# Optimization experiments

Hardware: AMD Instinct MI355X
Metric: run time of the kernel (lower is better)

The kernel has to match this reference:

```python
import jax, jax.numpy as jnp
import numpy as np

B, T, NW, NF = 4, 1, 1536, 16
N_CROSS = 400_000
N_EDGES = 1_600_000
C_OUT = 4
IN_DIM = 2 * NF + 2  # 34


def setup_inputs() -> dict:
    key = jax.random.key(0)
    ks = jax.random.split(key, 16)
    return {
        "first_wires": jax.random.normal(ks[0], (B, T, NW, NF), jnp.float32),
        "second_wires": jax.random.normal(ks[1], (B, T, NW, NF), jnp.float32),
        "crossings": jax.random.normal(ks[2], (N_CROSS, 2), jnp.float32),
        "bbox": jax.random.uniform(ks[3], (3,), jnp.float32) + 0.5,
        "edge_attr": jax.random.normal(ks[4], (N_EDGES, 4), jnp.float32),
        "indices": jax.random.randint(ks[5], (N_CROSS, 2), 0, NW),
        "edge_index": jax.random.randint(ks[6], (2, N_EDGES), 0, N_CROSS),
        "W": jax.random.normal(ks[7], (IN_DIM, C_OUT), jnp.float32) / np.sqrt(IN_DIM),
        "att_src": jax.random.normal(ks[8], (C_OUT,), jnp.float32),
        "att_dst": jax.random.normal(ks[9], (C_OUT,), jnp.float32),
        "W_e": jax.random.normal(ks[10], (4, C_OUT), jnp.float32) / 2.0,
        "att_edge": jax.random.normal(ks[11], (C_OUT,), jnp.float32),
        "bias": jnp.zeros((C_OUT,), jnp.float32),
        "w_mlp": jax.random.normal(ks[12], (C_OUT, 1), jnp.float32) / 2.0,
        "b_mlp": jnp.zeros((1,), jnp.float32),
    }


def reference(first_wires, second_wires, crossings, bbox, edge_attr,
              indices, edge_index, W, att_src, att_dst, W_e, att_edge,
              bias, w_mlp, b_mlp):
    b, t = first_wires.shape[0], first_wires.shape[1]
    n = indices.shape[0]
    # fill_window: gather wire features for each crossing and append normalized coords
    fw = first_wires[:, :, indices[:, 0], :]          # [B,T,N,NF]
    sw = second_wires[:, :, indices[:, 1], :]         # [B,T,N,NF]
    xc = crossings / jnp.linalg.norm(bbox)            # [N,2]
    xc = jnp.broadcast_to(xc[None, None], (b, t, n, 2))
    x = jnp.concatenate([fw, sw, xc], axis=-1)        # [B,T,N,2NF+2]
    x = x.reshape(b * t, n, -1)

    src, dst = edge_index[0], edge_index[1]
    h = x @ W                                          # [BT,N,C]
    a_e = (edge_attr @ W_e) @ att_edge                 # [E]

    def gat(hb):
        hs, hd = hb[src], hb[dst]                      # [E,C]
        logits = jax.nn.leaky_relu(hs @ att_src + hd @ att_dst + a_e, 0.2)
        m = jax.ops.segment_max(logits, dst, num_segments=n)
        ex = jnp.exp(logits - m[dst])
        den = jax.ops.segment_sum(ex, dst, num_segments=n)
        alpha = ex / (den[dst] + 1e-16)
        return jax.ops.segment_sum(alpha[:, None] * hs, dst, num_segments=n) + bias

    out = jax.vmap(gat)(h)                             # [BT,N,C]
    y = out @ w_mlp + b_mlp                            # [BT,N,1]
    return y.reshape(b, t, n, 1)
```

## Files before the change

kernel.cpp:

```cpp
#include <hip/hip_runtime.h>
#include <math.h>

#define BB 4
#define NWIRE 1536
#define NFEAT 16
#define BS 256
#define NBLK 256
#define DSHIFT 9
#define DPB (1 << DSHIFT)
#define MAXNB 1024

__global__ void k_wires(const float* __restrict__ fw, const float* __restrict__ sw,
                        const float* __restrict__ W, const float* __restrict__ att_src,
                        const float* __restrict__ att_dst, const float* __restrict__ wmlp,
                        float4* __restrict__ fwpre, float4* __restrict__ swpre) {
    int t = blockIdx.x * blockDim.x + threadIdx.x;
    if (t >= BB * NWIRE) return;
    const float* fp = fw + (size_t)t * NFEAT;
    const float* sp = sw + (size_t)t * NFEAT;
    float hf[4] = {0, 0, 0, 0}, hs[4] = {0, 0, 0, 0};
    #pragma unroll
    for (int k = 0; k < NFEAT; ++k) {
        float a = fp[k], b = sp[k];
        #pragma unroll
        for (int c = 0; c < 4; ++c) {
            hf[c] = fmaf(a, W[k * 4 + c], hf[c]);
            hs[c] = fmaf(b, W[(NFEAT + k) * 4 + c], hs[c]);
        }
    }
    float fs = 0, fd = 0, fq = 0, ss = 0, sd = 0, sq = 0;
    #pragma unroll
    for (int c = 0; c < 4; ++c) {
        float as = att_src[c], ad = att_dst[c], wm = wmlp[c];
        fs = fmaf(hf[c], as, fs); fd = fmaf(hf[c], ad, fd); fq = fmaf(hf[c], wm, fq);
        ss = fmaf(hs[c], as, ss); sd = fmaf(hs[c], ad, sd); sq = fmaf(hs[c], wm, sq);
    }
    fwpre[t] = make_float4(fs, fd, fq, 0.0f);
    swpre[t] = make_float4(ss, sd, sq, 0.0f);
}

__global__ void k_nodes(const int* __restrict__ indices, const float* __restrict__ crossings,
                        const float* __restrict__ bbox, const float* __restrict__ W,
                        const float* __restrict__ att_src, const float* __restrict__ att_dst,
                        const float* __restrict__ wmlp,
                        const float4* __restrict__ fwpre, const float4* __restrict__ swpre,
                        float4* __restrict__ srcdat4, float4* __restrict__ dstdat4, int n) {
    int i = blockIdx.x * blockDim.x + threadIdx.x;
    if (i >= n) return;
    float inv = rsqrtf(bbox[0] * bbox[0] + bbox[1] * bbox[1] + bbox[2] * bbox[2]);
    int i0 = indices[2 * i], i1 = indices[2 * i + 1];
    float x0 = crossings[2 * i] * inv, x1 = crossings[2 * i + 1] * inv;
    float xs = 0, xd = 0, xq = 0;
    #pragma unroll
    for (int c = 0; c < 4; ++c) {
        float hc = fmaf(x0, W[32 * 4 + c], x1 * W[33 * 4 + c]);
        xs = fmaf(hc, att_src[c], xs);
        xd = fmaf(hc, att_dst[c], xd);
        xq = fmaf(hc, wmlp[c], xq);
    }
    float4 f0 = fwpre[0 * NWIRE + i0], s0 = swpre[0 * NWIRE + i1];
    float4 f1 = fwpre[1 * NWIRE + i0], s1 = swpre[1 * NWIRE + i1];
    float4 f2 = fwpre[2 * NWIRE + i0], s2 = swpre[2 * NWIRE + i1];
    float4 f3 = fwpre[3 * NWIRE + i0], s3 = swpre[3 * NWIRE + i1];
    srcdat4[(size_t)i * 2] = make_float4(f0.x + s0.x + xs, f1.x + s1.x + xs,
                                         f2.x + s2.x + xs, f3.x + s3.x + xs);
    srcdat4[(size_t)i * 2 + 1] = make_float4(f0.z + s0.z + xq, f1.z + s1.z + xq,
                                             f2.z + s2.z + xq, f3.z + s3.z + xq);
    dstdat4[i] = make_float4(f0.y + s0.y + xd, f1.y + s1.y + xd,
                             f2.y + s2.y + xd, f3.y + s3.y + xd);
}

__global__ void k_binA1(const int* __restrict__ ei, int ne, int nb, int chunk,
                        int* __restrict__ bh) {
    __shared__ int lc[MAXNB];
    for (int i = threadIdx.x; i < nb; i += BS) lc[i] = 0;
    __syncthreads();
    int blk = blockIdx.x;
    int e0 = blk * chunk, e1 = min(e0 + chunk, ne);
    const int* dstp = ei + ne;
    for (int e = e0 + threadIdx.x; e < e1; e += BS)
        atomicAdd(&lc[dstp[e] >> DSHIFT], 1);
    __syncthreads();
    for (int b = threadIdx.x; b < nb; b += BS)
        bh[b * NBLK + blk] = lc[b];
}

__global__ void k_scanBlk(int* __restrict__ bh, int* __restrict__ btot, int nb) {
    int b = blockIdx.x * blockDim.x + threadIdx.x;
    if (b >= nb) return;
    int4* p = (int4*)(bh + (size_t)b * NBLK);
    int run = 0;
    #pragma unroll 4
    for (int k = 0; k < NBLK / 4; ++k) {
        int4 v = p[k];
        int4 o;
        o.x = run; run += v.x;
        o.y = run; run += v.y;
        o.z = run; run += v.z;
        o.w = run; run += v.w;
        p[k] = o;
    }
    btot[b] = run;
}

__global__ void k_scanBuck(const int* __restrict__ btot, int* __restrict__ bbase,
                           int nb, int ne) {
    __shared__ int sh[MAXNB];
    int t = threadIdx.x;
    int v = (t < nb) ? btot[t] : 0;
    sh[t] = v;
    __syncthreads();
    for (int ofs = 1; ofs < MAXNB; ofs <<= 1) {
        int u = (t >= ofs) ? sh[t - ofs] : 0;
        __syncthreads();
        sh[t] += u;
        __syncthreads();
    }
    if (t < nb) bbase[t] = sh[t] - v;
    if (t == 0) bbase[nb] = ne;
}

__global__ void k_binA2(const int* __restrict__ ei, const float* __restrict__ eattr,
                        const float* __restrict__ We, const float* __restrict__ att_edge,
                        const int* __restrict__ bh, const int* __restrict__ bbase,
                        int ne, int nb, int chunk, int2* __restrict__ recs) {
    __shared__ int curs[MAXNB];
    int blk = blockIdx.x;
    for (int b = threadIdx.x; b < nb; b += BS)
        curs[b] = bbase[b] + bh[b * NBLK + blk];
    __syncthreads();
    float v0 = fmaf(We[0], att_edge[0], fmaf(We[1], att_edge[1], fmaf(We[2], att_edge[2], We[3] * att_edge[3])));
    float v1 = fmaf(We[4], att_edge[0], fmaf(We[5], att_edge[1], fmaf(We[6], att_edge[2], We[7] * att_edge[3])));
    float v2 = fmaf(We[8], att_edge[0], fmaf(We[9], att_edge[1], fmaf(We[10], att_edge[2], We[11] * att_edge[3])));
    float v3 = fmaf(We[12], att_edge[0], fmaf(We[13], att_edge[1], fmaf(We[14], att_edge[2], We[15] * att_edge[3])));
    const int* srcp = ei;
    const int* dstp = ei + ne;
    int e0 = blk * chunk, e1 = min(e0 + chunk, ne);
    for (int e = e0 + threadIdx.x; e < e1; e += BS) {
        int s = srcp[e], d = dstp[e];
        const float4 ea = *(const float4*)(eattr + (size_t)e * 4);
        float ae = fmaf(ea.x, v0, fmaf(ea.y, v1, fmaf(ea.z, v2, ea.w * v3)));
        int b = d >> DSHIFT;
        int pos = atomicAdd(&curs[b], 1);
        recs[pos] = make_int2(((d & (DPB - 1)) << 19) | s, __float_as_int(ae));
    }
}

__global__ void k_gatB(const int2* __restrict__ recs, const int* __restrict__ bbase,
                       const float4* __restrict__ srcdat4, const float4* __restrict__ dstdat4,
                       const float* __restrict__ bias, const float* __restrict__ wmlp,
                       const float* __restrict__ bmlp, float* __restrict__ out, int n) {
    __shared__ float acc[DPB * 8];
    __shared__ float pds[DPB * 4];
    int b = blockIdx.x;
    int r0 = bbase[b], r1 = bbase[b + 1];
    int dbase = b << DSHIFT;
    int dmax = min(DPB, n - dbase);
    for (int i = threadIdx.x; i < DPB * 8; i += BS) acc[i] = 0.0f;
    for (int i = threadIdx.x; i < dmax; i += BS) {
        float4 pd = dstdat4[dbase + i];
        pds[i * 4]     = pd.x;
        pds[i * 4 + 1] = pd.y;
        pds[i * 4 + 2] = pd.z;
        pds[i * 4 + 3] = pd.w;
    }
    __syncthreads();
    for (int i = r0 + threadIdx.x; i < r1; i += BS) {
        int2 r = recs[i];
        int dlo = (unsigned)r.x >> 19;
        int src = r.x & 0x7FFFF;
        float ae = __int_as_float(r.y);
        float4 ps = srcdat4[(size_t)src * 2];
        float4 q  = srcdat4[(size_t)src * 2 + 1];
        float lg, ex;
        lg = ps.x + pds[dlo * 4]     + ae; lg = lg > 0.0f ? lg : 0.2f * lg; ex = expf(lg);
        atomicAdd(&acc[dlo * 8],     ex); atomicAdd(&acc[dlo * 8 + 1], ex * q.x);
        lg = ps.y + pds[dlo * 4 + 1] + ae; lg = lg > 0.0f ? lg : 0.2f * lg; ex = expf(lg);
        atomicAdd(&acc[dlo * 8 + 2], ex); atomicAdd(&acc[dlo * 8 + 3], ex * q.y);
        lg = ps.z + pds[dlo * 4 + 2] + ae; lg = lg > 0.0f ? lg : 0.2f * lg; ex = expf(lg);
        atomicAdd(&acc[dlo * 8 + 4], ex); atomicAdd(&acc[dlo * 8 + 5], ex * q.z);
        lg = ps.w + pds[dlo * 4 + 3] + ae; lg = lg > 0.0f ? lg : 0.2f * lg; ex = expf(lg);
        atomicAdd(&acc[dlo * 8 + 6], ex); atomicAdd(&acc[dlo * 8 + 7], ex * q.w);
    }
    __syncthreads();
    float cst = fmaf(bias[0], wmlp[0], fmaf(bias[1], wmlp[1], fmaf(bias[2], wmlp[2], bias[3] * wmlp[3]))) + bmlp[0];
    for (int i = threadIdx.x; i < dmax; i += BS) {
        int d = dbase + i;
        out[d]                 = acc[i * 8 + 1] / (acc[i * 8]     + 1e-16f) + cst;
        out[(size_t)n + d]     = acc[i * 8 + 3] / (acc[i * 8 + 2] + 1e-16f) + cst;
        out[(size_t)2 * n + d] = acc[i * 8 + 5] / (acc[i * 8 + 4] + 1e-16f) + cst;
        out[(size_t)3 * n + d] = acc[i * 8 + 7] / (acc[i * 8 + 6] + 1e-16f) + cst;
    }
}

extern "C" void kernel_launch(void* const* d_in, const int* in_sizes, int n_in,
                              void* d_out, int out_size, void* d_ws, size_t ws_size,
                              hipStream_t stream) {
    const float* first_wires  = (const float*)d_in[0];
    const float* second_wires = (const float*)d_in[1];
    const float* crossings    = (const float*)d_in[2];
    const float* bbox         = (const float*)d_in[3];
    const float* edge_attr    = (const float*)d_in[4];
    const int*   indices      = (const int*)d_in[5];
    const int*   edge_index   = (const int*)d_in[6];
    const float* W            = (const float*)d_in[7];
    const float* att_src      = (const float*)d_in[8];
    const float* att_dst      = (const float*)d_in[9];
    const float* W_e          = (const float*)d_in[10];
    const float* att_edge     = (const float*)d_in[11];
    const float* bias         = (const float*)d_in[12];
    const float* w_mlp        = (const float*)d_in[13];
    const float* b_mlp        = (const float*)d_in[14];
    float* out = (float*)d_out;

    const int n  = in_sizes[5] / 2;
    const int ne = in_sizes[6] / 2;
    const int nb = (n + DPB - 1) >> DSHIFT;
    const int chunk = (ne + NBLK - 1) / NBLK;

    char* ws = (char*)d_ws;
    size_t off = 0;
    float4* fwpre   = (float4*)(ws + off); off += (size_t)BB * NWIRE * 16;
    float4* swpre   = (float4*)(ws + off); off += (size_t)BB * NWIRE * 16;
    float4* srcdat4 = (float4*)(ws + off); off += (size_t)n * 32;
    float4* dstdat4 = (float4*)(ws + off); off += (size_t)n * 16;
    int*    bh      = (int*)(ws + off);    off += (size_t)nb * NBLK * 4;
    int*    btot    = (int*)(ws + off);    off += ((size_t)nb * 4 + 15) & ~15ull;
    int*    bbase   = (int*)(ws + off);    off += ((size_t)(nb + 1) * 4 + 15) & ~15ull;
    int2*   recs    = (int2*)(ws + off);   off += (size_t)ne * 8;

    hipLaunchKernelGGL(k_wires, dim3((BB * NWIRE + BS - 1) / BS), dim3(BS), 0, stream,
                       first_wires, second_wires, W, att_src, att_dst, w_mlp, fwpre, swpre);
    hipLaunchKernelGGL(k_nodes, dim3((n + BS - 1) / BS), dim3(BS), 0, stream,
                       indices, crossings, bbox, W, att_src, att_dst, w_mlp,
                       fwpre, swpre, srcdat4, dstdat4, n);
    hipLaunchKernelGGL(k_binA1, dim3(NBLK), dim3(BS), 0, stream,
                       edge_index, ne, nb, chunk, bh);
    hipLaunchKernelGGL(k_scanBlk, dim3((nb + 63) / 64), dim3(64), 0, stream,
                       bh, btot, nb);
    hipLaunchKernelGGL(k_scanBuck, dim3(1), dim3(MAXNB), 0, stream,
                       btot, bbase, nb, ne);
    hipLaunchKernelGGL(k_binA2, dim3(NBLK), dim3(BS), 0, stream,
                       edge_index, edge_attr, W_e, att_edge, bh, bbase, ne, nb, chunk, recs);
    hipLaunchKernelGGL(k_gatB, dim3(nb), dim3(BS), 0, stream,
                       recs, bbase, srcdat4, dstdat4, bias, w_mlp, b_mlp, out, n);
}
```

Measured before the change: 264.5 us.

## Halve destination bucket size, vectorize edge loads, transpose histogram layout, unroll GAT gathers

Halves the destination-bucket size so k_gatB launches twice as many blocks (about 1563 instead of 782) for more parallelism. The histogram is stored block-major so the per-block read and write become coalesced, while the column scan now reads with a stride. The edge binning kernels load src, dst and edge_attr four at a time as int4/float4, and the chunk size is rounded to a multiple of 4 to keep those loads aligned. The GAT kernel issues four record and source-feature gathers before processing them, to raise memory-level parallelism, and the bucket scan now handles two elements per thread.

```diff
diff --git a/kernel.cpp b/kernel.cpp
--- a/kernel.cpp
+++ b/kernel.cpp
@@ -6,9 +6,9 @@
 #define NFEAT 16
 #define BS 256
 #define NBLK 256
-#define DSHIFT 9
+#define DSHIFT 8
 #define DPB (1 << DSHIFT)
-#define MAXNB 1024
+#define MAXNB 2048
 
 __global__ void k_wires(const float* __restrict__ fw, const float* __restrict__ sw,
                         const float* __restrict__ W, const float* __restrict__ att_src,
@@ -48,8 +48,10 @@
     int i = blockIdx.x * blockDim.x + threadIdx.x;
     if (i >= n) return;
     float inv = rsqrtf(bbox[0] * bbox[0] + bbox[1] * bbox[1] + bbox[2] * bbox[2]);
-    int i0 = indices[2 * i], i1 = indices[2 * i + 1];
-    float x0 = crossings[2 * i] * inv, x1 = crossings[2 * i + 1] * inv;
+    int2 idx = ((const int2*)indices)[i];
+    float2 xc = ((const float2*)crossings)[i];
+    int i0 = idx.x, i1 = idx.y;
+    float x0 = xc.x * inv, x1 = xc.y * inv;
     float xs = 0, xd = 0, xq = 0;
     #pragma unroll
     for (int c = 0; c < 4; ++c) {
@@ -76,47 +78,61 @@
     for (int i = threadIdx.x; i < nb; i += BS) lc[i] = 0;
     __syncthreads();
     int blk = blockIdx.x;
+    const int* dstp = ei + ne;
     int e0 = blk * chunk, e1 = min(e0 + chunk, ne);
-    const int* dstp = ei + ne;
-    for (int e = e0 + threadIdx.x; e < e1; e += BS)
-        atomicAdd(&lc[dstp[e] >> DSHIFT], 1);
-    __syncthreads();
-    for (int b = threadIdx.x; b < nb; b += BS)
-        bh[b * NBLK + blk] = lc[b];
+    int e = e0 + threadIdx.x * 4;
+    for (; e + 3 < e1; e += BS * 4) {
+        int4 d4 = *(const int4*)(dstp + e);
+        atomicAdd(&lc[d4.x >> DSHIFT], 1);
+        atomicAdd(&lc[d4.y >> DSHIFT], 1);
+        atomicAdd(&lc[d4.z >> DSHIFT], 1);
+        atomicAdd(&lc[d4.w >> DSHIFT], 1);
+    }
+    for (; e < e1; e += BS * 4) {
+        int ke = min(e + 4, e1);
+        for (int k = e; k < ke; ++k) atomicAdd(&lc[dstp[k] >> DSHIFT], 1);
+    }
+    __syncthreads();
+    int* row = bh + (size_t)blk * nb;
+    for (int b = threadIdx.x; b < nb; b += BS) row[b] = lc[b];
 }
 
 __global__ void k_scanBlk(int* __restrict__ bh, int* __restrict__ btot, int nb) {
     int b = blockIdx.x * blockDim.x + threadIdx.x;
     if (b >= nb) return;
-    int4* p = (int4*)(bh + (size_t)b * NBLK);
     int run = 0;
-    #pragma unroll 4
-    for (int k = 0; k < NBLK / 4; ++k) {
-        int4 v = p[k];
-        int4 o;
-        o.x = run; run += v.x;
-        o.y = run; run += v.y;
-        o.z = run; run += v.z;
-        o.w = run; run += v.w;
-        p[k] = o;
+    for (int k0 = 0; k0 < NBLK; k0 += 8) {
+        int v[8];
+        #pragma unroll
+        for (int j = 0; j < 8; ++j) v[j] = bh[(size_t)(k0 + j) * nb + b];
+        #pragma unroll
+        for (int j = 0; j < 8; ++j) {
+            int t = v[j];
+            bh[(size_t)(k0 + j) * nb + b] = run;
+            run += t;
+        }
     }
     btot[b] = run;
 }
 
 __global__ void k_scanBuck(const int* __restrict__ btot, int* __restrict__ bbase,
                            int nb, int ne) {
-    __shared__ int sh[MAXNB];
+    __shared__ int sh[1024];
     int t = threadIdx.x;
-    int v = (t < nb) ? btot[t] : 0;
-    sh[t] = v;
-    __syncthreads();
-    for (int ofs = 1; ofs < MAXNB; ofs <<= 1) {
+    int i0 = 2 * t, i1 = 2 * t + 1;
+    int a = (i0 < nb) ? btot[i0] : 0;
+    int b = (i1 < nb) ? btot[i1] : 0;
+    sh[t] = a + b;
+    __syncthreads();
+    for (int ofs = 1; ofs < 1024; ofs <<= 1) {
         int u = (t >= ofs) ? sh[t - ofs] : 0;
         __syncthreads();
         sh[t] += u;
         __syncthreads();
     }
-    if (t < nb) bbase[t] = sh[t] - v;
+    int excl = sh[t] - (a + b);
+    if (i0 < nb) bbase[i0] = excl;
+    if (i1 < nb) bbase[i1] = excl + a;
     if (t == 0) bbase[nb] = ne;
 }
 
@@ -126,8 +142,9 @@
                         int ne, int nb, int chunk, int2* __restrict__ recs) {
     __shared__ int curs[MAXNB];
     int blk = blockIdx.x;
+    const int* row = bh + (size_t)blk * nb;
     for (int b = threadIdx.x; b < nb; b += BS)
-        curs[b] = bbase[b] + bh[b * NBLK + blk];
+        curs[b] = bbase[b] + row[b];
     __syncthreads();
     float v0 = fmaf(We[0], att_edge[0], fmaf(We[1], att_edge[1], fmaf(We[2], att_edge[2], We[3] * att_edge[3])));
     float v1 = fmaf(We[4], att_edge[0], fmaf(We[5], att_edge[1], fmaf(We[6], att_edge[2], We[7] * att_edge[3])));
@@ -135,21 +152,58 @@
     float v3 = fmaf(We[12], att_edge[0], fmaf(We[13], att_edge[1], fmaf(We[14], att_edge[2], We[15] * att_edge[3])));
     const int* srcp = ei;
     const int* dstp = ei + ne;
+    const float4* ea4 = (const float4*)eattr;
     int e0 = blk * chunk, e1 = min(e0 + chunk, ne);
-    for (int e = e0 + threadIdx.x; e < e1; e += BS) {
-        int s = srcp[e], d = dstp[e];
-        const float4 ea = *(const float4*)(eattr + (size_t)e * 4);
-        float ae = fmaf(ea.x, v0, fmaf(ea.y, v1, fmaf(ea.z, v2, ea.w * v3)));
-        int b = d >> DSHIFT;
-        int pos = atomicAdd(&curs[b], 1);
-        recs[pos] = make_int2(((d & (DPB - 1)) << 19) | s, __float_as_int(ae));
-    }
-}
-
-__global__ void k_gatB(const int2* __restrict__ recs, const int* __restrict__ bbase,
-                       const float4* __restrict__ srcdat4, const float4* __restrict__ dstdat4,
-                       const float* __restrict__ bias, const float* __restrict__ wmlp,
-                       const float* __restrict__ bmlp, float* __restrict__ out, int n) {
+    int e = e0 + threadIdx.x * 4;
+    for (; e + 3 < e1; e += BS * 4) {
+        int4 s4 = *(const int4*)(srcp + e);
+        int4 d4 = *(const int4*)(dstp + e);
+        float4 a0 = ea4[e], a1 = ea4[e + 1], a2 = ea4[e + 2], a3 = ea4[e + 3];
+        float ae0 = fmaf(a0.x, v0, fmaf(a0.y, v1, fmaf(a0.z, v2, a0.w * v3)));
+        float ae1 = fmaf(a1.x, v0, fmaf(a1.y, v1, fmaf(a1.z, v2, a1.w * v3)));
+        float ae2 = fmaf(a2.x, v0, fmaf(a2.y, v1, fmaf(a2.z, v2, a2.w * v3)));
+        float ae3 = fmaf(a3.x, v0, fmaf(a3.y, v1, fmaf(a3.z, v2, a3.w * v3)));
+        int p0 = atomicAdd(&curs[d4.x >> DSHIFT], 1);
+        int p1 = atomicAdd(&curs[d4.y >> DSHIFT], 1);
+        int p2 = atomicAdd(&curs[d4.z >> DSHIFT], 1);
+        int p3 = atomicAdd(&curs[d4.w >> DSHIFT], 1);
+        recs[p0] = make_int2(((d4.x & (DPB - 1)) << 19) | s4.x, __float_as_int(ae0));
+        recs[p1] = make_int2(((d4.y & (DPB - 1)) << 19) | s4.y, __float_as_int(ae1));
+        recs[p2] = make_int2(((d4.z & (DPB - 1)) << 19) | s4.z, __float_as_int(ae2));
+        recs[p3] = make_int2(((d4.w & (DPB - 1)) << 19) | s4.w, __float_as_int(ae3));
+    }
+    for (; e < e1; e += BS * 4) {
+        int ke = min(e + 4, e1);
+        for (int k = e; k < ke; ++k) {
+            int s = srcp[k], d = dstp[k];
+            float4 ea = ea4[k];
+            float ae = fmaf(ea.x, v0, fmaf(ea.y, v1, fmaf(ea.z, v2, ea.w * v3)));
+            int pos = atomicAdd(&curs[d >> DSHIFT], 1);
+            recs[pos] = make_int2(((d & (DPB - 1)) << 19) | s, __float_as_int(ae));
+        }
+    }
+}
+
+__device__ __forceinline__ void gat_proc(int2 r, float4 ps, float4 q,
+                                         float* acc, const float* pds) {
+    int dlo = (unsigned)r.x >> 19;
+    float ae = __int_as_float(r.y);
+    float lg, ex;
+    lg = ps.x + pds[dlo * 4]     + ae; lg = lg > 0.0f ? lg : 0.2f * lg; ex = expf(lg);
+    atomicAdd(&acc[dlo * 8],     ex); atomicAdd(&acc[dlo * 8 + 1], ex * q.x);
+    lg = ps.y + pds[dlo * 4 + 1] + ae; lg = lg > 0.0f ? lg : 0.2f * lg; ex = expf(lg);
+    atomicAdd(&acc[dlo * 8 + 2], ex); atomicAdd(&acc[dlo * 8 + 3], ex * q.y);
+    lg = ps.z + pds[dlo * 4 + 2] + ae; lg = lg > 0.0f ? lg : 0.2f * lg; ex = expf(lg);
+    atomicAdd(&acc[dlo * 8 + 4], ex); atomicAdd(&acc[dlo * 8 + 5], ex * q.z);
+    lg = ps.w + pds[dlo * 4 + 3] + ae; lg = lg > 0.0f ? lg : 0.2f * lg; ex = expf(lg);
+    atomicAdd(&acc[dlo * 8 + 6], ex); atomicAdd(&acc[dlo * 8 + 7], ex * q.w);
+}
+
+__global__ void __launch_bounds__(BS)
+k_gatB(const int2* __restrict__ recs, const int* __restrict__ bbase,
+       const float4* __restrict__ srcdat4, const float4* __restrict__ dstdat4,
+       const float* __restrict__ bias, const float* __restrict__ wmlp,
+       const float* __restrict__ bmlp, float* __restrict__ out, int n) {
     __shared__ float acc[DPB * 8];
     __shared__ float pds[DPB * 4];
     int b = blockIdx.x;
@@ -165,31 +219,33 @@
         pds[i * 4 + 3] = pd.w;
     }
     __syncthreads();
-    for (int i = r0 + threadIdx.x; i < r1; i += BS) {
+    int i = r0 + threadIdx.x;
+    for (; i + 3 * BS < r1; i += 4 * BS) {
+        int2 ra = recs[i], rb = recs[i + BS], rc = recs[i + 2 * BS], rd = recs[i + 3 * BS];
+        int sa = ra.x & 0x7FFFF, sb = rb.x & 0x7FFFF;
+        int sc = rc.x & 0x7FFFF, sd = rd.x & 0x7FFFF;
+        float4 Pa = srcdat4[(size_t)sa * 2], Qa = srcdat4[(size_t)sa * 2 + 1];
+        float4 Pb = srcdat4[(size_t)sb * 2], Qb = srcdat4[(size_t)sb * 2 + 1];
+        float4 Pc = srcdat4[(size_t)sc * 2], Qc = srcdat4[(size_t)sc * 2 + 1];
+        float4 Pd = srcdat4[(size_t)sd * 2], Qd = srcdat4[(size_t)sd * 2 + 1];
+        gat_proc(ra, Pa, Qa, acc, pds);
+        gat_proc(rb, Pb, Qb, acc, pds);
+        gat_proc(rc, Pc, Qc, acc, pds);
+        gat_proc(rd, Pd, Qd, acc, pds);
+    }
+    for (; i < r1; i += BS) {
         int2 r = recs[i];
-        int dlo = (unsigned)r.x >> 19;
-        int src = r.x & 0x7FFFF;
-        float ae = __int_as_float(r.y);
-        float4 ps = srcdat4[(size_t)src * 2];
-        float4 q  = srcdat4[(size_t)src * 2 + 1];
-        float lg, ex;
-        lg = ps.x + pds[dlo * 4]     + ae; lg = lg > 0.0f ? lg : 0.2f * lg; ex = expf(lg);
-        atomicAdd(&acc[dlo * 8],     ex); atomicAdd(&acc[dlo * 8 + 1], ex * q.x);
-        lg = ps.y + pds[dlo * 4 + 1] + ae; lg = lg > 0.0f ? lg : 0.2f * lg; ex = expf(lg);
-        atomicAdd(&acc[dlo * 8 + 2], ex); atomicAdd(&acc[dlo * 8 + 3], ex * q.y);
-        lg = ps.z + pds[dlo * 4 + 2] + ae; lg = lg > 0.0f ? lg : 0.2f * lg; ex = expf(lg);
-        atomicAdd(&acc[dlo * 8 + 4], ex); atomicAdd(&acc[dlo * 8 + 5], ex * q.z);
-        lg = ps.w + pds[dlo * 4 + 3] + ae; lg = lg > 0.0f ? lg : 0.2f * lg; ex = expf(lg);
-        atomicAdd(&acc[dlo * 8 + 6], ex); atomicAdd(&acc[dlo * 8 + 7], ex * q.w);
+        int s = r.x & 0x7FFFF;
+        gat_proc(r, srcdat4[(size_t)s * 2], srcdat4[(size_t)s * 2 + 1], acc, pds);
     }
     __syncthreads();
     float cst = fmaf(bias[0], wmlp[0], fmaf(bias[1], wmlp[1], fmaf(bias[2], wmlp[2], bias[3] * wmlp[3]))) + bmlp[0];
-    for (int i = threadIdx.x; i < dmax; i += BS) {
-        int d = dbase + i;
-        out[d]                 = acc[i * 8 + 1] / (acc[i * 8]     + 1e-16f) + cst;
-        out[(size_t)n + d]     = acc[i * 8 + 3] / (acc[i * 8 + 2] + 1e-16f) + cst;
-        out[(size_t)2 * n + d] = acc[i * 8 + 5] / (acc[i * 8 + 4] + 1e-16f) + cst;
-        out[(size_t)3 * n + d] = acc[i * 8 + 7] / (acc[i * 8 + 6] + 1e-16f) + cst;
+    for (int i2 = threadIdx.x; i2 < dmax; i2 += BS) {
+        int d = dbase + i2;
+        out[d]                 = acc[i2 * 8 + 1] / (acc[i2 * 8]     + 1e-16f) + cst;
+        out[(size_t)n + d]     = acc[i2 * 8 + 3] / (acc[i2 * 8 + 2] + 1e-16f) + cst;
+        out[(size_t)2 * n + d] = acc[i2 * 8 + 5] / (acc[i2 * 8 + 4] + 1e-16f) + cst;
+        out[(size_t)3 * n + d] = acc[i2 * 8 + 7] / (acc[i2 * 8 + 6] + 1e-16f) + cst;
     }
 }
 
@@ -216,7 +272,7 @@
     const int n  = in_sizes[5] / 2;
     const int ne = in_sizes[6] / 2;
     const int nb = (n + DPB - 1) >> DSHIFT;
-    const int chunk = (ne + NBLK - 1) / NBLK;
+    const int chunk = (((ne + NBLK - 1) / NBLK) + 3) & ~3;
 
     char* ws = (char*)d_ws;
     size_t off = 0;
@@ -238,7 +294,7 @@
                        edge_index, ne, nb, chunk, bh);
     hipLaunchKernelGGL(k_scanBlk, dim3((nb + 63) / 64), dim3(64), 0, stream,
                        bh, btot, nb);
-    hipLaunchKernelGGL(k_scanBuck, dim3(1), dim3(MAXNB), 0, stream,
+    hipLaunchKernelGGL(k_scanBuck, dim3(1), dim3(1024), 0, stream,
                        btot, bbase, nb, ne);
     hipLaunchKernelGGL(k_binA2, dim3(NBLK), dim3(BS), 0, stream,
                        edge_index, edge_attr, W_e, att_edge, bh, bbase, ne, nb, chunk, recs);
```

After: 257.9 us. -2.5%, faster.
